# Kernel tuning notes

Measured on AMD Instinct MI355X. Metric: run time of the kernel, lower is better.

Reference implementation:

```python
import jax, jax.numpy as jnp
import numpy as np

H, F = 4, 32          # GAT heads, per-head channels (= hidden_dim)
NEG_ATT = 0.2         # GATConv attention leaky_relu slope (PyG default)
NEG_ACT = 0.01        # F.leaky_relu / nn.LeakyReLU default slope
NUM_ID = 9            # len(map_candid_to_numid)


def _leaky(x, s):
    return jnp.where(x >= 0, x, s * x)


def gat_conv(x, src, dst, n, W, att_src, att_dst, bias):
    # PyG GATConv(heads=4, concat=False): softmax over in-edges per dst node,
    # weighted scatter-add, mean over heads, then bias.
    h = (x @ W).reshape(n, H, F)
    a_s = jnp.einsum('nhf,hf->nh', h, att_src)
    a_d = jnp.einsum('nhf,hf->nh', h, att_dst)
    e = _leaky(a_s[src] + a_d[dst], NEG_ATT)                        # [E,H]
    m = jax.ops.segment_max(e, dst, num_segments=n)                 # stable softmax max
    m = jnp.where(jnp.isfinite(m), m, 0.0)
    ex = jnp.exp(e - m[dst])
    denom = jax.ops.segment_sum(ex, dst, num_segments=n) + 1e-16    # PyG softmax eps
    alpha = ex / denom[dst]
    out = jax.ops.segment_sum(alpha[:, :, None] * h[src], dst, num_segments=n)
    return out.mean(axis=1) + bias


def _gat_params(k, din):
    k1, k2, k3 = jax.random.split(k, 3)
    return (jax.random.normal(k1, (din, H * F), jnp.float32) * np.float32(1.0 / np.sqrt(din)),
            jax.random.normal(k2, (H, F), jnp.float32) * 0.1,
            jax.random.normal(k3, (H, F), jnp.float32) * 0.1,
            jnp.zeros((F,), jnp.float32))


def setup_inputs() -> dict:
    key = jax.random.key(0)
    ks = jax.random.split(key, 20)
    N, E, D = 100000, 800000, 3
    x = jax.random.normal(ks[0], (N, D), jnp.float32)
    x = x.at[: N // 2, 0].set(0.0)  # towers: x[:,0] == 0
    edge_index = jax.random.randint(ks[1], (2, E), 0, N, dtype=jnp.int64)
    edge_attr = jax.random.uniform(ks[2], (E, 1), dtype=jnp.float32)
    inp = {'x': x, 'edge_index': edge_index, 'edge_attr': edge_attr}
    for i, din in enumerate([D, F, F]):
        W, a_s, a_d, b = _gat_params(ks[3 + i], din)
        inp[f'W{i+1}'] = W; inp[f'a_src{i+1}'] = a_s
        inp[f'a_dst{i+1}'] = a_d; inp[f'b{i+1}'] = b
    mlp_dims = [(D + F, F), (F, F), (F, F), (F, F), (F, NUM_ID + 3)]
    for i, (di, do) in enumerate(mlp_dims):
        k1, k2 = jax.random.split(ks[10 + i])
        inp[f'mW{i+1}'] = jax.random.normal(k1, (di, do), jnp.float32) * np.float32(1.0 / np.sqrt(di))
        inp[f'mb{i+1}'] = jax.random.normal(k2, (do,), jnp.float32) * 0.01
    return inp


def reference(x, edge_index, edge_attr, W1, a_src1, a_dst1, b1,
              W2, a_src2, a_dst2, b2, W3, a_src3, a_dst3, b3,
              mW1, mb1, mW2, mb2, mW3, mb3, mW4, mb4, mW5, mb5):
    # edge_attr / batch are read but unused by the torch forward.
    n = x.shape[0]
    loops = jnp.arange(n, dtype=edge_index.dtype)  # add_self_loops=True
    src = jnp.concatenate([edge_index[0], loops])
    dst = jnp.concatenate([edge_index[1], loops])
    x1 = _leaky(gat_conv(x, src, dst, n, W1, a_src1, a_dst1, b1), NEG_ACT)
    x2 = _leaky(gat_conv(x1, src, dst, n, W2, a_src2, a_dst2, b2), NEG_ACT)
    x3 = _leaky(gat_conv(x2, src, dst, n, W3, a_src3, a_dst3, b3), NEG_ACT)
    h = jnp.concatenate([x, x3], axis=-1)
    for W, b in [(mW1, mb1), (mW2, mb2), (mW3, mb3), (mW4, mb4)]:
        h = _leaky(h @ W + b, NEG_ACT)  # Dropout(0.5) is identity in eval
    cands = h @ mW5 + mb5               # [N, 12]
    mask_tower = x[:, 0] == 0           # data-dependent split (eager-mode indexing)
    ct = cands[mask_tower]
    ck = cands[~mask_tower]
    return (ct[:, :NUM_ID], ck[:, :NUM_ID], ct[:, NUM_ID:], ck[:, NUM_ID:])
```

## Files before the change

### kernel.cpp

```cpp
#include <hip/hip_runtime.h>
#include <hip/hip_bf16.h>

#define DEV __device__ __forceinline__

DEV float bf2f(__hip_bfloat16 v) { return __bfloat162float(v); }

typedef unsigned long long ull;

__global__ void k_detect_zero(const unsigned short* xr, int nprobe, int* flag,
                              int* cnt, int N) {
    int i = blockIdx.x * 256 + threadIdx.x;
    if (i < N) cnt[i] = 0;
    if (blockIdx.x == 0) {
        __shared__ int red[256];
        int t = threadIdx.x, bad = 0;
        for (int j = t; j < nprobe; j += 256) {
            unsigned e = (xr[j] >> 7) & 0xFF;
            if (e >= 0x8F) bad++;
        }
        red[t] = bad; __syncthreads();
        for (int o = 128; o > 0; o >>= 1) { if (t < o) red[t] += red[t + o]; __syncthreads(); }
        if (t == 0) flag[0] = (red[0] > 256) ? 1 : 0;
    }
}

struct Seg  { const void* src; int off; int len; };
struct Segs { Seg s[22]; };

__global__ void k_fused(const void* xsrc, int nx3, Segs segs, float* canon,
                        const int* flag, const int* eidx, int E, int N,
                        int* cnt, int* msk, int* rank) {
    int f32 = flag[0];
    int t = threadIdx.x, b = blockIdx.x;
    if (b < 64) {
        for (int i = b * 256 + t; i < nx3; i += 64 * 256) {
            float v = f32 ? ((const float*)xsrc)[i] : bf2f(((const __hip_bfloat16*)xsrc)[i]);
            if (!(v == v) || fabsf(v) > 1e30f) v = 0.f;
            canon[i] = v;
            if (i % 3 == 0) msk[i / 3] = (v == 0.0f) ? 1 : 0;
        }
    } else if (b < 86) {
        Seg sg = segs.s[b - 64];
        for (int i = t; i < sg.len; i += 256) {
            float v = f32 ? ((const float*)sg.src)[i] : bf2f(((const __hip_bfloat16*)sg.src)[i]);
            if (!(v == v) || fabsf(v) > 1e30f) v = 0.f;
            canon[sg.off + i] = v;
        }
    } else {
        int e = (b - 86) * 256 + t;
        if (e < E) {
            int d = eidx[E + e];
            if ((unsigned)d < (unsigned)N) {
                int p = atomicAdd(&cnt[d], 1);
                rank[e] = p;
            }
        }
    }
}


DEV ull packval(const int* cnt, const int* msk, int i) {
    return ((ull)(unsigned)msk[i] << 32) | (unsigned)(cnt[i] + 1);
}

__global__ void k_scan_partial64(const int* __restrict__ cnt, const int* __restrict__ msk,
                                 int n, ull* __restrict__ partials) {
    __shared__ ull red[256];
    int t = threadIdx.x, b = blockIdx.x;
    int base = b * 1024 + t * 4;
    ull s = 0;
    #pragma unroll
    for (int j = 0; j < 4; j++) { int i = base + j; if (i < n) s += packval(cnt, msk, i); }
    red[t] = s; __syncthreads();
    for (int o = 128; o > 0; o >>= 1) { if (t < o) red[t] += red[t + o]; __syncthreads(); }
    if (t == 0) partials[b] = red[0];
}

__global__ void k_scan_mid64(ull* partials, int nb, int* offN, int* totals) {
    __shared__ ull sh[256];
    int t = threadIdx.x;
    ull carry = 0;
    for (int base = 0; base < nb; base += 256) {
        int i = base + t;
        ull v = (i < nb) ? partials[i] : 0;
        sh[t] = v; __syncthreads();
        for (int o = 1; o < 256; o <<= 1) {
            ull x = (t >= o) ? sh[t - o] : 0;
            __syncthreads();
            sh[t] += x;
            __syncthreads();
        }
        if (i < nb) partials[i] = carry + sh[t] - v;
        ull tot = sh[255];
        __syncthreads();
        carry += tot;
    }
    if (t == 0) { *offN = (int)(carry & 0xffffffffu); *totals = (int)(carry >> 32); }
}

__global__ void k_scan_final64(const int* __restrict__ cnt, int* __restrict__ msk, int n,
                               const ull* __restrict__ partials,
                               int* __restrict__ off) {
    __shared__ ull sums[256];
    int t = threadIdx.x, b = blockIdx.x;
    int base = b * 1024 + t * 4;
    ull v0 = 0, v1 = 0, v2 = 0, v3 = 0;
    if (base     < n) v0 = packval(cnt, msk, base);
    if (base + 1 < n) v1 = packval(cnt, msk, base + 1);
    if (base + 2 < n) v2 = packval(cnt, msk, base + 2);
    if (base + 3 < n) v3 = packval(cnt, msk, base + 3);
    ull s = v0 + v1 + v2 + v3;
    sums[t] = s; __syncthreads();
    for (int o = 1; o < 256; o <<= 1) {
        ull x = (t >= o) ? sums[t - o] : 0;
        __syncthreads();
        sums[t] += x;
        __syncthreads();
    }
    ull run = partials[b] + (sums[t] - s);
    #pragma unroll
    for (int j = 0; j < 4; j++) {
        int i = base + j;
        if (i < n) {
            off[i] = (int)(run & 0xffffffffu);
            msk[i] = (int)(run >> 32);
            run += (j == 0 ? v0 : j == 1 ? v1 : j == 2 ? v2 : v3);
        }
    }
}


__global__ __launch_bounds__(256) void k_fill_node1(
    const int* __restrict__ eidx, const int* __restrict__ rank, int E, int N,
    const int* __restrict__ off, int* __restrict__ esrc,
    const float* __restrict__ xF, const float* __restrict__ W,
    const float* __restrict__ atS, const float* __restrict__ atD,
    __hip_bfloat162* __restrict__ h2, float* __restrict__ as_, float* __restrict__ ad_,
    int gfill) {
    __shared__ float xl[64 * 4];
    int b = blockIdx.x;
    if (b < gfill) {
        int e = b * 256 + threadIdx.x;
        if (e < E) {
            int s = eidx[e], d = eidx[E + e];
            if ((unsigned)d < (unsigned)N && (unsigned)s < (unsigned)N)
                esrc[off[d] + rank[e]] = s;
        } else if (e < E + N) {
            int i = e - E;
            esrc[off[i + 1] - 1] = i;
        }
        return;
    }
    int t = threadIdx.x, lane = t & 63, w = t >> 6;
    int nblk = (b - gfill) * 64;
    int cnt = N - nblk; if (cnt > 64) cnt = 64;

    if (t < 64) xl[t * 4 + 3] = 0.f;
    for (int i = t; i < cnt * 3; i += 256) xl[(i / 3) * 4 + (i % 3)] = xF[(size_t)nblk * 3 + i];

    const float2* W2 = (const float2*)W;
    float2 Wr0 = W2[0 * 64 + lane], Wr1 = W2[1 * 64 + lane], Wr2 = W2[2 * 64 + lane];
    float2 aSp = ((const float2*)atS)[lane];
    float2 aDp = ((const float2*)atD)[lane];
    int hd = lane >> 4;
    __syncthreads();

    for (int i = 0; i < 16; i++) {
        int n = nblk + w * 16 + i;
        if (n >= N) break;
        float4 xv = ((const float4*)xl)[w * 16 + i];
        float acc0 = xv.x * Wr0.x + xv.y * Wr1.x + xv.z * Wr2.x;
        float acc1 = xv.x * Wr0.y + xv.y * Wr1.y + xv.z * Wr2.y;
        __hip_bfloat162 hv; hv.x = __float2bfloat16(acc0); hv.y = __float2bfloat16(acc1);
        h2[(size_t)n * 64 + lane] = hv;
        float p = acc0 * aSp.x + acc1 * aSp.y;
        float q = acc0 * aDp.x + acc1 * aDp.y;
        #pragma unroll
        for (int o = 1; o < 16; o <<= 1) { p += __shfl_xor(p, o, 64); q += __shfl_xor(q, o, 64); }
        if ((lane & 15) == 0) { as_[n * 4 + hd] = p; ad_[n * 4 + hd] = q; }
    }
}


__global__ __launch_bounds__(256) void k_node_mid(
    const float* __restrict__ xin, const float* __restrict__ W,
    const float* __restrict__ atS, const float* __restrict__ atD,
    int N, __hip_bfloat162* __restrict__ h2, float* __restrict__ as_, float* __restrict__ ad_) {
    __shared__ float xl[64 * 32];
    int t = threadIdx.x, lane = t & 63, w = t >> 6;
    int nblk = blockIdx.x * 64;
    int cnt = N - nblk; if (cnt > 64) cnt = 64;

    {
        const float4* g4 = (const float4*)(xin + (size_t)nblk * 32);
        float4* l4 = (float4*)xl;
        int lim = cnt * 8;
        if (t < lim) l4[t] = g4[t];
        int t2 = t + 256;
        if (t2 < lim) l4[t2] = g4[t2];
    }

    const float2* W2 = (const float2*)W;
    float2 Wr[32];
    #pragma unroll
    for (int k = 0; k < 32; k++) Wr[k] = W2[k * 64 + lane];
    float2 aSp = ((const float2*)atS)[lane];
    float2 aDp = ((const float2*)atD)[lane];
    int hd = lane >> 4;
    __syncthreads();

    for (int i = 0; i < 16; i++) {
        int n = nblk + w * 16 + i;
        if (n >= N) break;
        const float4* xv4 = (const float4*)&xl[(w * 16 + i) * 32];
        float acc0 = 0.f, acc1 = 0.f;
        #pragma unroll
        for (int kk = 0; kk < 8; kk++) {
            float4 xv = xv4[kk];
            acc0 += xv.x * Wr[4*kk+0].x; acc1 += xv.x * Wr[4*kk+0].y;
            acc0 += xv.y * Wr[4*kk+1].x; acc1 += xv.y * Wr[4*kk+1].y;
            acc0 += xv.z * Wr[4*kk+2].x; acc1 += xv.z * Wr[4*kk+2].y;
            acc0 += xv.w * Wr[4*kk+3].x; acc1 += xv.w * Wr[4*kk+3].y;
        }
        __hip_bfloat162 hv; hv.x = __float2bfloat16(acc0); hv.y = __float2bfloat16(acc1);
        h2[(size_t)n * 64 + lane] = hv;
        float p = acc0 * aSp.x + acc1 * aSp.y;
        float q = acc0 * aDp.x + acc1 * aDp.y;
        #pragma unroll
        for (int o = 1; o < 16; o <<= 1) { p += __shfl_xor(p, o, 64); q += __shfl_xor(q, o, 64); }
        if ((lane & 15) == 0) { as_[n * 4 + hd] = p; ad_[n * 4 + hd] = q; }
    }
}


constexpr int FCAP  = 64;
constexpr int FCAPP = 68;

__global__ __launch_bounds__(256) void k_edge(
    const __hip_bfloat162* __restrict__ h2, const float* __restrict__ as_,
    const float* __restrict__ ad_, const int* __restrict__ off,
    const int* __restrict__ esrc, const float* __restrict__ bias,
    int N, float* __restrict__ xout) {
    __shared__ float alphaS[4][4 * FCAPP];
    __shared__ int   srcS[4][FCAP];
    int t = threadIdx.x, lane = t & 63, w = t >> 6;
    int n = blockIdx.x * 4 + w;
    if (n >= N) return;
    int beg = off[n], end = off[n + 1];
    int deg = end - beg;
    float4 adn = ((const float4*)ad_)[n];
    const float4* as4 = (const float4*)as_;
    int hd = lane >> 4;

    float acc0 = 0.f, acc1 = 0.f;

    if (deg <= 16) {
        int e = lane >> 2, h = lane & 3;
        int s_e = n;
        float v = -1e30f;
        if (e < deg) {
            int s = esrc[beg + e];
            if ((unsigned)s < (unsigned)N) {
                s_e = s;
                float asv = as_[s * 4 + h];
                float adv = h == 0 ? adn.x : h == 1 ? adn.y : h == 2 ? adn.z : adn.w;
                v = asv + adv; v = v >= 0.f ? v : 0.2f * v;
            }
        }
        float m = v;
        #pragma unroll
        for (int o = 4; o < 64; o <<= 1) m = fmaxf(m, __shfl_xor(m, o, 64));
        float ex = (v > -1e29f) ? __expf(v - m) : 0.f;
        float ssum = ex;
        #pragma unroll
        for (int o = 4; o < 64; o <<= 1) ssum += __shfl_xor(ssum, o, 64);
        float inv = 1.f / (ssum + 1e-16f);
        float invH = __shfl(inv, hd, 64);

        #pragma unroll
        for (int c = 0; c < 4; c++) {
            if (4 * c < deg) {
                float w0 = __shfl(ex, 16 * c + 0  + hd, 64) * invH;
                float w1 = __shfl(ex, 16 * c + 4  + hd, 64) * invH;
                float w2 = __shfl(ex, 16 * c + 8  + hd, 64) * invH;
                float w3 = __shfl(ex, 16 * c + 12 + hd, 64) * invH;
                int s0 = __shfl(s_e, 16 * c + 0, 64);
                int s1 = __shfl(s_e, 16 * c + 4, 64);
                int s2 = __shfl(s_e, 16 * c + 8, 64);
                int s3 = __shfl(s_e, 16 * c + 12, 64);
                __hip_bfloat162 g0 = h2[(size_t)s0 * 64 + lane];
                __hip_bfloat162 g1 = h2[(size_t)s1 * 64 + lane];
                __hip_bfloat162 g2 = h2[(size_t)s2 * 64 + lane];
                __hip_bfloat162 g3 = h2[(size_t)s3 * 64 + lane];
                acc0 += w0 * bf2f(g0.x) + w1 * bf2f(g1.x) + w2 * bf2f(g2.x) + w3 * bf2f(g3.x);
                acc1 += w0 * bf2f(g0.y) + w1 * bf2f(g1.y) + w2 * bf2f(g2.y) + w3 * bf2f(g3.y);
            }
        }
    } else {
        bool fits = (deg <= FCAP);
        float m0 = -1e30f, m1 = -1e30f, m2 = -1e30f, m3 = -1e30f;
        for (int e = beg + lane; e < end; e += 64) {
            int s = esrc[e];
            if ((unsigned)s >= (unsigned)N) continue;
            float4 a = as4[s];
            float v0 = a.x + adn.x; v0 = v0 >= 0.f ? v0 : 0.2f * v0;
            float v1 = a.y + adn.y; v1 = v1 >= 0.f ? v1 : 0.2f * v1;
            float v2 = a.z + adn.z; v2 = v2 >= 0.f ? v2 : 0.2f * v2;
            float v3 = a.w + adn.w; v3 = v3 >= 0.f ? v3 : 0.2f * v3;
            m0 = fmaxf(m0, v0); m1 = fmaxf(m1, v1); m2 = fmaxf(m2, v2); m3 = fmaxf(m3, v3);
        }
        #pragma unroll
        for (int o = 1; o < 64; o <<= 1) {
            m0 = fmaxf(m0, __shfl_xor(m0, o, 64));
            m1 = fmaxf(m1, __shfl_xor(m1, o, 64));
            m2 = fmaxf(m2, __shfl_xor(m2, o, 64));
            m3 = fmaxf(m3, __shfl_xor(m3, o, 64));
        }
        float s0 = 0.f, s1 = 0.f, s2 = 0.f, s3 = 0.f;
        for (int e = beg + lane; e < end; e += 64) {
            int s = esrc[e];
            bool ok = (unsigned)s < (unsigned)N;
            float4 a = ok ? as4[s] : make_float4(-1e30f, -1e30f, -1e30f, -1e30f);
            float v0 = a.x + adn.x; v0 = v0 >= 0.f ? v0 : 0.2f * v0;
            float v1 = a.y + adn.y; v1 = v1 >= 0.f ? v1 : 0.2f * v1;
            float v2 = a.z + adn.z; v2 = v2 >= 0.f ? v2 : 0.2f * v2;
            float v3 = a.w + adn.w; v3 = v3 >= 0.f ? v3 : 0.2f * v3;
            float e0 = __expf(v0 - m0), e1 = __expf(v1 - m1);
            float e2 = __expf(v2 - m2), e3 = __expf(v3 - m3);
            s0 += e0; s1 += e1; s2 += e2; s3 += e3;
            if (fits) {
                int i = e - beg;
                srcS[w][i] = ok ? s : n;
                alphaS[w][0 * FCAPP + i] = e0;
                alphaS[w][1 * FCAPP + i] = e1;
                alphaS[w][2 * FCAPP + i] = e2;
                alphaS[w][3 * FCAPP + i] = e3;
            }
        }
        #pragma unroll
        for (int o = 1; o < 64; o <<= 1) {
            s0 += __shfl_xor(s0, o, 64); s1 += __shfl_xor(s1, o, 64);
            s2 += __shfl_xor(s2, o, 64); s3 += __shfl_xor(s3, o, 64);
        }
        float i0 = 1.f / (s0 + 1e-16f), i1 = 1.f / (s1 + 1e-16f);
        float i2 = 1.f / (s2 + 1e-16f), i3 = 1.f / (s3 + 1e-16f);
        float invH = hd == 0 ? i0 : hd == 1 ? i1 : hd == 2 ? i2 : i3;
        if (fits) {
            for (int i = 0; i < deg; i++) {
                int s = srcS[w][i];
                float wt = alphaS[w][hd * FCAPP + i] * invH;
                __hip_bfloat162 hv = h2[(size_t)s * 64 + lane];
                acc0 += wt * bf2f(hv.x);
                acc1 += wt * bf2f(hv.y);
            }
        } else {
            float mH  = hd == 0 ? m0 : hd == 1 ? m1 : hd == 2 ? m2 : m3;
            float adH = hd == 0 ? adn.x : hd == 1 ? adn.y : hd == 2 ? adn.z : adn.w;
            for (int e = beg; e < end; e++) {
                int s = esrc[e];
                if ((unsigned)s >= (unsigned)N) continue;
                float4 a = as4[s];
                float aH = hd == 0 ? a.x : hd == 1 ? a.y : hd == 2 ? a.z : a.w;
                float v = aH + adH; v = v >= 0.f ? v : 0.2f * v;
                float wt = __expf(v - mH) * invH;
                __hip_bfloat162 hv = h2[(size_t)s * 64 + lane];
                acc0 += wt * bf2f(hv.x);
                acc1 += wt * bf2f(hv.y);
            }
        }
    }
    acc0 += __shfl_xor(acc0, 16, 64); acc0 += __shfl_xor(acc0, 32, 64);
    acc1 += __shfl_xor(acc1, 16, 64); acc1 += __shfl_xor(acc1, 32, 64);
    if (lane < 16) {
        float o0 = acc0 * 0.25f + bias[2 * lane];     o0 = o0 >= 0.f ? o0 : 0.01f * o0;
        float o1 = acc1 * 0.25f + bias[2 * lane + 1]; o1 = o1 >= 0.f ? o1 : 0.01f * o1;
        ((float2*)xout)[(size_t)n * 16 + lane] = make_float2(o0, o1);
    }
}


__global__ __launch_bounds__(128) void k_mlp(
    const float* __restrict__ xF, const float* __restrict__ x3,
    const float* __restrict__ mW1, const float* __restrict__ mb1,
    const float* __restrict__ mW2, const float* __restrict__ mb2,
    const float* __restrict__ mW3, const float* __restrict__ mb3,
    const float* __restrict__ mW4, const float* __restrict__ mb4,
    const float* __restrict__ mW5, const float* __restrict__ mb5,
    const int* __restrict__ smask, const int* __restrict__ totals,
    const int* __restrict__ flag, int N, void* __restrict__ out) {
    __shared__ float W1[35 * 32], W2[1024], W3[1024], W4[1024], W5[32 * 12];
    __shared__ float B1[32], B2[32], B3[32], B4[32], B5[12];
    __shared__ float actA[35 * 128];
    __shared__ float actB[32 * 128];
    int t = threadIdx.x;
    for (int i = t; i < 1120; i += 128) W1[i] = mW1[i];
    for (int i = t; i < 1024; i += 128) { W2[i] = mW2[i]; W3[i] = mW3[i]; W4[i] = mW4[i]; }
    for (int i = t; i < 384; i += 128) W5[i] = mW5[i];
    if (t < 32) { B1[t] = mb1[t]; B2[t] = mb2[t]; B3[t] = mb3[t]; B4[t] = mb4[t]; }
    if (t < 12) B5[t] = mb5[t];
    __syncthreads();

    int n = blockIdx.x * 128 + t;
    bool alive = (n < N);
    float x0 = 0.f;
    if (alive) {
        x0 = xF[n * 3 + 0];
        actA[0 * 128 + t] = x0;
        actA[1 * 128 + t] = xF[n * 3 + 1];
        actA[2 * 128 + t] = xF[n * 3 + 2];
        for (int i = 0; i < 32; i++) actA[(3 + i) * 128 + t] = x3[(size_t)n * 32 + i];
    }

    float acc[32];

    #pragma unroll
    for (int o = 0; o < 32; o++) acc[o] = B1[o];
    #pragma unroll 2
    for (int i = 0; i < 35; i++) {
        float ai = actA[i * 128 + t];
        const float4* w4 = (const float4*)&W1[i * 32];
        #pragma unroll
        for (int q = 0; q < 8; q++) {
            float4 w = w4[q];
            acc[q*4+0] += ai * w.x; acc[q*4+1] += ai * w.y;
            acc[q*4+2] += ai * w.z; acc[q*4+3] += ai * w.w;
        }
    }
    #pragma unroll
    for (int o = 0; o < 32; o++) { float v = acc[o]; actB[o * 128 + t] = (v >= 0.f ? v : 0.01f * v); }

    #pragma unroll
    for (int o = 0; o < 32; o++) acc[o] = B2[o];
    #pragma unroll 2
    for (int i = 0; i < 32; i++) {
        float ai = actB[i * 128 + t];
        const float4* w4 = (const float4*)&W2[i * 32];
        #pragma unroll
        for (int q = 0; q < 8; q++) {
            float4 w = w4[q];
            acc[q*4+0] += ai * w.x; acc[q*4+1] += ai * w.y;
            acc[q*4+2] += ai * w.z; acc[q*4+3] += ai * w.w;
        }
    }
    #pragma unroll
    for (int o = 0; o < 32; o++) { float v = acc[o]; actA[o * 128 + t] = (v >= 0.f ? v : 0.01f * v); }

    #pragma unroll
    for (int o = 0; o < 32; o++) acc[o] = B3[o];
    #pragma unroll 2
    for (int i = 0; i < 32; i++) {
        float ai = actA[i * 128 + t];
        const float4* w4 = (const float4*)&W3[i * 32];
        #pragma unroll
        for (int q = 0; q < 8; q++) {
            float4 w = w4[q];
            acc[q*4+0] += ai * w.x; acc[q*4+1] += ai * w.y;
            acc[q*4+2] += ai * w.z; acc[q*4+3] += ai * w.w;
        }
    }
    #pragma unroll
    for (int o = 0; o < 32; o++) { float v = acc[o]; actB[o * 128 + t] = (v >= 0.f ? v : 0.01f * v); }

    #pragma unroll
    for (int o = 0; o < 32; o++) acc[o] = B4[o];
    #pragma unroll 2
    for (int i = 0; i < 32; i++) {
        float ai = actB[i * 128 + t];
        const float4* w4 = (const float4*)&W4[i * 32];
        #pragma unroll
        for (int q = 0; q < 8; q++) {
            float4 w = w4[q];
            acc[q*4+0] += ai * w.x; acc[q*4+1] += ai * w.y;
            acc[q*4+2] += ai * w.z; acc[q*4+3] += ai * w.w;
        }
    }
    #pragma unroll
    for (int o = 0; o < 32; o++) { float v = acc[o]; actA[o * 128 + t] = (v >= 0.f ? v : 0.01f * v); }

    float d[12];
    #pragma unroll
    for (int o = 0; o < 12; o++) d[o] = B5[o];
    #pragma unroll 2
    for (int i = 0; i < 32; i++) {
        float ai = actA[i * 128 + t];
        const float4* w4 = (const float4*)&W5[i * 12];
        #pragma unroll
        for (int q = 0; q < 3; q++) {
            float4 w = w4[q];
            d[q*4+0] += ai * w.x; d[q*4+1] += ai * w.y;
            d[q*4+2] += ai * w.z; d[q*4+3] += ai * w.w;
        }
    }
    if (!alive) return;
    #pragma unroll
    for (int o = 0; o < 12; o++) if (!(d[o] == d[o])) d[o] = 0.f;

    bool tower = (x0 == 0.0f);
    int r = smask[n];
    int Nt = *totals;
    int f32o = *flag;
    int base9, base3, rr;
    if (tower) { rr = r;     base9 = 0;      base3 = 9 * N; }
    else       { rr = n - r; base9 = 9 * Nt; base3 = 9 * N + 3 * Nt; }
    if (f32o) {
        float* o = (float*)out;
        #pragma unroll
        for (int j = 0; j < 9; j++) o[base9 + rr * 9 + j] = d[j];
        #pragma unroll
        for (int j = 0; j < 3; j++) o[base3 + rr * 3 + j] = d[9 + j];
    } else {
        __hip_bfloat16* o = (__hip_bfloat16*)out;
        #pragma unroll
        for (int j = 0; j < 9; j++) o[base9 + rr * 9 + j] = __float2bfloat16(d[j]);
        #pragma unroll
        for (int j = 0; j < 3; j++) o[base3 + rr * 3 + j] = __float2bfloat16(d[9 + j]);
    }
}


extern "C" void kernel_launch(void* const* d_in, const int* in_sizes, int n_in,
                              void* d_out, int out_size, void* d_ws, size_t ws_size,
                              hipStream_t stream) {
    const void* xraw = d_in[0];
    const int*  eidx = (const int*)d_in[1];

    int N  = in_sizes[0] / 3;
    int E  = in_sizes[1] / 2;
    int EE = E + N;

    Segs segs;
    int coff[22];
    int canonN = 3 * N;
    for (int i = 3; i <= 24; i++) {
        int a = i - 3;
        segs.s[a].src = d_in[i];
        segs.s[a].off = canonN;
        segs.s[a].len = in_sizes[i];
        coff[a] = canonN;
        canonN += in_sizes[i];
    }

    auto alignv = [](size_t v, size_t a) { return (v + a - 1) & ~(a - 1); };
    char* base = (char*)d_ws;
    size_t o = 0;
    float* canon = (float*)(base + o); o = alignv(o + (size_t)canonN * 4, 16);
    int* flag     = (int*)(base + o); o = alignv(o + 16, 16);
    ull* partials = (ull*)(base + o); o = alignv(o + 1024 * 8, 16);
    int* totals   = (int*)(base + o); o = alignv(o + 16, 16);
    int* off      = (int*)(base + o); o = alignv(o + (size_t)(N + 1) * 4, 16);
    int* cnt      = (int*)(base + o); o = alignv(o + (size_t)N * 4, 16);
    int* esrc     = (int*)(base + o); o = alignv(o + (size_t)EE * 4, 16);
    int* rank     = (int*)(base + o); o = alignv(o + (size_t)E * 4, 16);
    int* msk      = (int*)(base + o); o = alignv(o + (size_t)N * 4, 256);
    __hip_bfloat162* h2 = (__hip_bfloat162*)(base + o); o = alignv(o + (size_t)N * 64 * 4, 16);
    float* xb  = (float*)(base + o); o = alignv(o + (size_t)N * 32 * 4, 16);
    float* as_ = (float*)(base + o); o = alignv(o + (size_t)N * 16, 16);
    float* ad_ = (float*)(base + o);

    int nb = (N + 1023) / 1024;
    int gN = (N + 255) / 256;
    int g4 = (N + 3) / 4;
    int g64 = (N + 63) / 64;
    int gM = (N + 127) / 128;
    int gfill = (EE + 255) / 256;

    int nprobe = in_sizes[0] < 4096 ? in_sizes[0] : 4096;
    k_detect_zero<<<gN, 256, 0, stream>>>((const unsigned short*)xraw, nprobe, flag, cnt, N);
    k_fused<<<86 + (E + 255) / 256, 256, 0, stream>>>(xraw, 3 * N, segs, canon, flag,
                                                      eidx, E, N, cnt, msk, rank);
    k_scan_partial64<<<nb, 256, 0, stream>>>(cnt, msk, N, partials);
    k_scan_mid64<<<1, 256, 0, stream>>>(partials, nb, off + N, totals);
    k_scan_final64<<<nb, 256, 0, stream>>>(cnt, msk, N, partials, off);

    float* xF = canon;
    const float* W1  = canon + coff[0];  const float* aS1 = canon + coff[1];
    const float* aD1 = canon + coff[2];  const float* b1  = canon + coff[3];
    const float* W2  = canon + coff[4];  const float* aS2 = canon + coff[5];
    const float* aD2 = canon + coff[6];  const float* b2  = canon + coff[7];
    const float* W3  = canon + coff[8];  const float* aS3 = canon + coff[9];
    const float* aD3 = canon + coff[10]; const float* b3  = canon + coff[11];

    k_fill_node1<<<gfill + g64, 256, 0, stream>>>(eidx, rank, E, N, off, esrc,
                                                  xF, W1, aS1, aD1, h2, as_, ad_, gfill);
    k_edge<<<g4, 256, 0, stream>>>(h2, as_, ad_, off, esrc, b1, N, xb);
    k_node_mid<<<g64, 256, 0, stream>>>(xb, W2, aS2, aD2, N, h2, as_, ad_);
    k_edge<<<g4, 256, 0, stream>>>(h2, as_, ad_, off, esrc, b2, N, xb);
    k_node_mid<<<g64, 256, 0, stream>>>(xb, W3, aS3, aD3, N, h2, as_, ad_);
    k_edge<<<g4, 256, 0, stream>>>(h2, as_, ad_, off, esrc, b3, N, xb);

    k_mlp<<<gM, 128, 0, stream>>>(xF, xb,
        canon + coff[12], canon + coff[13], canon + coff[14], canon + coff[15],
        canon + coff[16], canon + coff[17], canon + coff[18], canon + coff[19],
        canon + coff[20], canon + coff[21], msk, totals, flag, N, d_out);
}
```

Measured before the change: 437.6 us.

## Fuse GAT edge aggregation with next layer's node transform using ping-pong buffers

```diff
diff --git a/kernel.cpp b/kernel.cpp
--- a/kernel.cpp
+++ b/kernel.cpp
@@ -236,23 +236,16 @@
 constexpr int FCAP  = 64;
 constexpr int FCAPP = 68;
 
-__global__ __launch_bounds__(256) void k_edge(
-    const __hip_bfloat162* __restrict__ h2, const float* __restrict__ as_,
-    const float* __restrict__ ad_, const int* __restrict__ off,
-    const int* __restrict__ esrc, const float* __restrict__ bias,
-    int N, float* __restrict__ xout) {
-    __shared__ float alphaS[4][4 * FCAPP];
-    __shared__ int   srcS[4][FCAP];
-    int t = threadIdx.x, lane = t & 63, w = t >> 6;
-    int n = blockIdx.x * 4 + w;
-    if (n >= N) return;
-    int beg = off[n], end = off[n + 1];
-    int deg = end - beg;
+template<typename LDSA, typename LDSS>
+DEV void edge_aggregate(const __hip_bfloat162* __restrict__ h2,
+                        const float* __restrict__ as_, const float* __restrict__ ad_,
+                        const int* __restrict__ esrc, int beg, int deg, int n, int N,
+                        int lane, int hd, LDSA& alphaS, LDSS& srcS,
+                        float& acc0, float& acc1) {
     float4 adn = ((const float4*)ad_)[n];
     const float4* as4 = (const float4*)as_;
-    int hd = lane >> 4;
-
-    float acc0 = 0.f, acc1 = 0.f;
+    int end = beg + deg;
+    acc0 = 0.f; acc1 = 0.f;
 
     if (deg <= 16) {
         int e = lane >> 2, h = lane & 3;
@@ -280,10 +273,10 @@
         #pragma unroll
         for (int c = 0; c < 4; c++) {
             if (4 * c < deg) {
-                float w0 = __shfl(ex, 16 * c + 0  + hd, 64) * invH;
-                float w1 = __shfl(ex, 16 * c + 4  + hd, 64) * invH;
-                float w2 = __shfl(ex, 16 * c + 8  + hd, 64) * invH;
-                float w3 = __shfl(ex, 16 * c + 12 + hd, 64) * invH;
+                float w0 = __shfl(ex, 16 * c + 0  + hd, 64);
+                float w1 = __shfl(ex, 16 * c + 4  + hd, 64);
+                float w2 = __shfl(ex, 16 * c + 8  + hd, 64);
+                float w3 = __shfl(ex, 16 * c + 12 + hd, 64);
                 int s0 = __shfl(s_e, 16 * c + 0, 64);
                 int s1 = __shfl(s_e, 16 * c + 4, 64);
                 int s2 = __shfl(s_e, 16 * c + 8, 64);
@@ -296,6 +289,7 @@
                 acc1 += w0 * bf2f(g0.y) + w1 * bf2f(g1.y) + w2 * bf2f(g2.y) + w3 * bf2f(g3.y);
             }
         }
+        acc0 *= invH; acc1 *= invH;
     } else {
         bool fits = (deg <= FCAP);
         float m0 = -1e30f, m1 = -1e30f, m2 = -1e30f, m3 = -1e30f;
@@ -330,11 +324,11 @@
             s0 += e0; s1 += e1; s2 += e2; s3 += e3;
             if (fits) {
                 int i = e - beg;
-                srcS[w][i] = ok ? s : n;
-                alphaS[w][0 * FCAPP + i] = e0;
-                alphaS[w][1 * FCAPP + i] = e1;
-                alphaS[w][2 * FCAPP + i] = e2;
-                alphaS[w][3 * FCAPP + i] = e3;
+                srcS[i] = ok ? s : n;
+                alphaS[0 * FCAPP + i] = e0;
+                alphaS[1 * FCAPP + i] = e1;
+                alphaS[2 * FCAPP + i] = e2;
+                alphaS[3 * FCAPP + i] = e3;
             }
         }
         #pragma unroll
@@ -347,8 +341,8 @@
         float invH = hd == 0 ? i0 : hd == 1 ? i1 : hd == 2 ? i2 : i3;
         if (fits) {
             for (int i = 0; i < deg; i++) {
-                int s = srcS[w][i];
-                float wt = alphaS[w][hd * FCAPP + i] * invH;
+                int s = srcS[i];
+                float wt = alphaS[hd * FCAPP + i];
                 __hip_bfloat162 hv = h2[(size_t)s * 64 + lane];
                 acc0 += wt * bf2f(hv.x);
                 acc1 += wt * bf2f(hv.y);
@@ -362,13 +356,32 @@
                 float4 a = as4[s];
                 float aH = hd == 0 ? a.x : hd == 1 ? a.y : hd == 2 ? a.z : a.w;
                 float v = aH + adH; v = v >= 0.f ? v : 0.2f * v;
-                float wt = __expf(v - mH) * invH;
+                float wt = __expf(v - mH);
                 __hip_bfloat162 hv = h2[(size_t)s * 64 + lane];
                 acc0 += wt * bf2f(hv.x);
                 acc1 += wt * bf2f(hv.y);
             }
         }
-    }
+        acc0 *= invH; acc1 *= invH;
+    }
+}
+
+
+__global__ __launch_bounds__(256) void k_edge(
+    const __hip_bfloat162* __restrict__ h2, const float* __restrict__ as_,
+    const float* __restrict__ ad_, const int* __restrict__ off,
+    const int* __restrict__ esrc, const float* __restrict__ bias,
+    int N, float* __restrict__ xout) {
+    __shared__ float alphaS[4][4 * FCAPP];
+    __shared__ int   srcS[4][FCAP];
+    int t = threadIdx.x, lane = t & 63, w = t >> 6;
+    int n = blockIdx.x * 4 + w;
+    if (n >= N) return;
+    int beg = off[n], deg = off[n + 1] - beg;
+    int hd = lane >> 4;
+    float acc0, acc1;
+    edge_aggregate(h2, as_, ad_, esrc, beg, deg, n, N, lane, hd,
+                   alphaS[w], srcS[w], acc0, acc1);
     acc0 += __shfl_xor(acc0, 16, 64); acc0 += __shfl_xor(acc0, 32, 64);
     acc1 += __shfl_xor(acc1, 16, 64); acc1 += __shfl_xor(acc1, 32, 64);
     if (lane < 16) {
@@ -376,6 +389,57 @@
         float o1 = acc1 * 0.25f + bias[2 * lane + 1]; o1 = o1 >= 0.f ? o1 : 0.01f * o1;
         ((float2*)xout)[(size_t)n * 16 + lane] = make_float2(o0, o1);
     }
+}
+
+
+__global__ __launch_bounds__(256) void k_edge_node(
+    const __hip_bfloat162* __restrict__ h2r, const float* __restrict__ as_,
+    const float* __restrict__ ad_, const int* __restrict__ off,
+    const int* __restrict__ esrc, const float* __restrict__ bias, int N,
+    const float* __restrict__ Wn, const float* __restrict__ atSn,
+    const float* __restrict__ atDn,
+    __hip_bfloat162* __restrict__ h2w, float* __restrict__ as_w,
+    float* __restrict__ ad_w) {
+    __shared__ float alphaS[4][4 * FCAPP];
+    __shared__ int   srcS[4][FCAP];
+    __shared__ __align__(16) float xw[4 * 32];
+    int t = threadIdx.x, lane = t & 63, w = t >> 6;
+    int n = blockIdx.x * 4 + w;
+    if (n >= N) return;
+    int beg = off[n], deg = off[n + 1] - beg;
+    int hd = lane >> 4;
+    float acc0, acc1;
+    edge_aggregate(h2r, as_, ad_, esrc, beg, deg, n, N, lane, hd,
+                   alphaS[w], srcS[w], acc0, acc1);
+    acc0 += __shfl_xor(acc0, 16, 64); acc0 += __shfl_xor(acc0, 32, 64);
+    acc1 += __shfl_xor(acc1, 16, 64); acc1 += __shfl_xor(acc1, 32, 64);
+    if (lane < 16) {
+        float o0 = acc0 * 0.25f + bias[2 * lane];     o0 = o0 >= 0.f ? o0 : 0.01f * o0;
+        float o1 = acc1 * 0.25f + bias[2 * lane + 1]; o1 = o1 >= 0.f ? o1 : 0.01f * o1;
+        ((float2*)&xw[w * 32])[lane] = make_float2(o0, o1);
+    }
+    const float2* Wn2 = (const float2*)Wn;
+    float2 aSp = ((const float2*)atSn)[lane];
+    float2 aDp = ((const float2*)atDn)[lane];
+    const float4* xv4 = (const float4*)&xw[w * 32];
+    float na0 = 0.f, na1 = 0.f;
+    #pragma unroll
+    for (int kk = 0; kk < 8; kk++) {
+        float4 xv = xv4[kk];
+        float2 w0 = Wn2[(4*kk+0) * 64 + lane];
+        float2 w1 = Wn2[(4*kk+1) * 64 + lane];
+        float2 w2 = Wn2[(4*kk+2) * 64 + lane];
+        float2 w3 = Wn2[(4*kk+3) * 64 + lane];
+        na0 += xv.x * w0.x + xv.y * w1.x + xv.z * w2.x + xv.w * w3.x;
+        na1 += xv.x * w0.y + xv.y * w1.y + xv.z * w2.y + xv.w * w3.y;
+    }
+    __hip_bfloat162 hv; hv.x = __float2bfloat16(na0); hv.y = __float2bfloat16(na1);
+    h2w[(size_t)n * 64 + lane] = hv;
+    float p = na0 * aSp.x + na1 * aSp.y;
+    float q = na0 * aDp.x + na1 * aDp.y;
+    #pragma unroll
+    for (int o = 1; o < 16; o <<= 1) { p += __shfl_xor(p, o, 64); q += __shfl_xor(q, o, 64); }
+    if ((lane & 15) == 0) { as_w[n * 4 + hd] = p; ad_w[n * 4 + hd] = q; }
 }
 
 
@@ -552,10 +616,17 @@
     int* esrc     = (int*)(base + o); o = alignv(o + (size_t)EE * 4, 16);
     int* rank     = (int*)(base + o); o = alignv(o + (size_t)E * 4, 16);
     int* msk      = (int*)(base + o); o = alignv(o + (size_t)N * 4, 256);
-    __hip_bfloat162* h2 = (__hip_bfloat162*)(base + o); o = alignv(o + (size_t)N * 64 * 4, 16);
-    float* xb  = (float*)(base + o); o = alignv(o + (size_t)N * 32 * 4, 16);
-    float* as_ = (float*)(base + o); o = alignv(o + (size_t)N * 16, 16);
-    float* ad_ = (float*)(base + o);
+    __hip_bfloat162* h2A = (__hip_bfloat162*)(base + o); o = alignv(o + (size_t)N * 64 * 4, 16);
+    float* xb   = (float*)(base + o); o = alignv(o + (size_t)N * 32 * 4, 16);
+    float* asA  = (float*)(base + o); o = alignv(o + (size_t)N * 16, 16);
+    float* adA  = (float*)(base + o); o = alignv(o + (size_t)N * 16, 16);
+    size_t base_need = o;
+    __hip_bfloat162* h2B = (__hip_bfloat162*)(base + o); o = alignv(o + (size_t)N * 64 * 4, 16);
+    float* asB  = (float*)(base + o); o = alignv(o + (size_t)N * 16, 16);
+    float* adB  = (float*)(base + o); o = alignv(o + (size_t)N * 16, 16);
+    size_t fused_need = o;
+    bool use_fused = (ws_size >= fused_need);
+    (void)base_need;
 
     int nb = (N + 1023) / 1024;
     int gN = (N + 255) / 256;
@@ -581,12 +652,20 @@
     const float* aD3 = canon + coff[10]; const float* b3  = canon + coff[11];
 
     k_fill_node1<<<gfill + g64, 256, 0, stream>>>(eidx, rank, E, N, off, esrc,
-                                                  xF, W1, aS1, aD1, h2, as_, ad_, gfill);
-    k_edge<<<g4, 256, 0, stream>>>(h2, as_, ad_, off, esrc, b1, N, xb);
-    k_node_mid<<<g64, 256, 0, stream>>>(xb, W2, aS2, aD2, N, h2, as_, ad_);
-    k_edge<<<g4, 256, 0, stream>>>(h2, as_, ad_, off, esrc, b2, N, xb);
-    k_node_mid<<<g64, 256, 0, stream>>>(xb, W3, aS3, aD3, N, h2, as_, ad_);
-    k_edge<<<g4, 256, 0, stream>>>(h2, as_, ad_, off, esrc, b3, N, xb);
+                                                  xF, W1, aS1, aD1, h2A, asA, adA, gfill);
+    if (use_fused) {
+        k_edge_node<<<g4, 256, 0, stream>>>(h2A, asA, adA, off, esrc, b1, N,
+                                            W2, aS2, aD2, h2B, asB, adB);
+        k_edge_node<<<g4, 256, 0, stream>>>(h2B, asB, adB, off, esrc, b2, N,
+                                            W3, aS3, aD3, h2A, asA, adA);
+        k_edge<<<g4, 256, 0, stream>>>(h2A, asA, adA, off, esrc, b3, N, xb);
+    } else {
+        k_edge<<<g4, 256, 0, stream>>>(h2A, asA, adA, off, esrc, b1, N, xb);
+        k_node_mid<<<g64, 256, 0, stream>>>(xb, W2, aS2, aD2, N, h2A, asA, adA);
+        k_edge<<<g4, 256, 0, stream>>>(h2A, asA, adA, off, esrc, b2, N, xb);
+        k_node_mid<<<g64, 256, 0, stream>>>(xb, W3, aS3, aD3, N, h2A, asA, adA);
+        k_edge<<<g4, 256, 0, stream>>>(h2A, asA, adA, off, esrc, b3, N, xb);
+    }
 
     k_mlp<<<gM, 128, 0, stream>>>(xF, xb,
         canon + coff[12], canon + coff[13], canon + coff[14], canon + coff[15],
```

Result: slower. 526.8 us (+20.4%).
